# Kernel tuning notes

Measured on AMD Instinct MI355X. Metric: run time of the kernel, lower is better.

## Reference

```python
import jax, jax.numpy as jnp
import numpy as np
import math

# IPA hyperparameters (AlphaFold2 / ProtSeed defaults)
H, C, PQ, PV = 12, 16, 4, 8
CS, CZ = 384, 128
INF, EPS = 1e5, 1e-8
CAT = H * (CZ + C + 4 * PV)  # 2112


def setup_inputs() -> dict:
    key = jax.random.key(0)
    ks = jax.random.split(key, 20)
    B, N = 1, 512
    s = jax.random.normal(ks[0], (B, N, CS), jnp.float32)
    z = jax.random.normal(ks[1], (B, N, N, CZ), jnp.float32)
    # valid rotation matrices via QR of random gaussians
    rot = jnp.linalg.qr(jax.random.normal(ks[2], (B, N, 3, 3), jnp.float32))[0]
    trans = jax.random.normal(ks[3], (B, N, 3), jnp.float32)
    mask = jnp.ones((B, N), jnp.float32)
    sc = 0.02
    params = {
        'w_q': jax.random.normal(ks[4], (CS, H * C), jnp.float32) * sc,
        'b_q': jnp.zeros((H * C,), jnp.float32),
        'w_kv': jax.random.normal(ks[5], (CS, 2 * H * C), jnp.float32) * sc,
        'b_kv': jnp.zeros((2 * H * C,), jnp.float32),
        'w_qp': jax.random.normal(ks[6], (CS, H * PQ * 3), jnp.float32) * sc,
        'b_qp': jnp.zeros((H * PQ * 3,), jnp.float32),
        'w_kvp': jax.random.normal(ks[7], (CS, H * (PQ + PV) * 3), jnp.float32) * sc,
        'b_kvp': jnp.zeros((H * (PQ + PV) * 3,), jnp.float32),
        'w_b': jax.random.normal(ks[8], (CZ, H), jnp.float32) * sc,
        'b_b': jnp.zeros((H,), jnp.float32),
        'head_weights': jnp.full((H,), 0.5414, jnp.float32),  # softplus^-1(1)
        'w_out': jax.random.normal(ks[9], (CAT, CS), jnp.float32) * sc,
        'b_out': jnp.zeros((CS,), jnp.float32),
    }
    return {'s': s, 'z': z, 'rot': rot, 'trans': trans, 'mask': mask, **params}


def reference(s, z, rot, trans, mask, w_q, b_q, w_kv, b_kv, w_qp, b_qp,
              w_kvp, b_kvp, w_b, b_b, head_weights, w_out, b_out):
    B, N, _ = s.shape
    w_c = math.sqrt(1.0 / (3 * C))
    w_l = math.sqrt(1.0 / 3)
    w_p = math.sqrt(1.0 / (3 * (PQ * 9.0 / 2)))

    # scalar q/k/v: [B,N,H,C]
    q = (s @ w_q + b_q).reshape(B, N, H, C)
    kv = (s @ w_kv + b_kv).reshape(B, N, H, 2 * C)
    k, v = kv[..., :C], kv[..., C:]

    # point q/k/v in global frame. torch splits the projection into 3 chunks
    # (x,y,z) along the channel dim then stacks -> [B,N,H*P,3]
    def to_pts(w, b, p):
        pts = jnp.stack(jnp.split(s @ w + b, 3, axis=-1), axis=-1)  # [B,N,H*p,3]
        pts = jnp.einsum('bnij,bnpj->bnpi', rot, pts) + trans[:, :, None, :]
        return pts.reshape(B, N, H, p, 3)

    q_pts = to_pts(w_qp, b_qp, PQ)
    kv_pts = to_pts(w_kvp, b_kvp, PQ + PV)
    k_pts, v_pts = kv_pts[..., :PQ, :], kv_pts[..., PQ:, :]

    # pair bias [B,N,N,H]
    bias = z @ w_b + b_b

    # scalar attention logits [B,H,i,j]
    a = jnp.einsum('bihc,bjhc->bhij', q, k) * w_c
    a = a + w_l * jnp.transpose(bias, (0, 3, 1, 2))

    # point-distance term: [B,i,j,H,PQ]
    d2 = jnp.sum((q_pts[:, :, None] - k_pts[:, None]) ** 2, axis=-1)
    hw = jax.nn.softplus(head_weights) * w_p
    pt_att = -0.5 * jnp.sum(d2 * hw[None, None, None, :, None], axis=-1)  # [B,i,j,H]
    a = a + jnp.transpose(pt_att, (0, 3, 1, 2))

    sq_mask = INF * (mask[:, :, None] * mask[:, None, :] - 1.0)  # [B,i,j]
    a = jax.nn.softmax(a + sq_mask[:, None], axis=-1)  # [B,H,i,j]

    # scalar output [B,N,H*C]
    o = jnp.einsum('bhij,bjhc->bihc', a, v).reshape(B, N, H * C)

    # point output, mapped back to local frames: [B,i,H,PV,3]
    o_pt = jnp.einsum('bhij,bjhpx->bihpx', a, v_pts)
    o_pt = jnp.einsum('bnji,bnhpj->bnhpi', rot, o_pt - trans[:, :, None, None, :])
    o_pt_norm = jnp.sqrt(jnp.sum(o_pt ** 2, axis=-1) + EPS).reshape(B, N, H * PV)
    o_pt = o_pt.reshape(B, N, H * PV, 3)

    # pair output [B,N,H*CZ]
    o_pair = jnp.einsum('bhij,bijc->bihc', a, z).reshape(B, N, H * CZ)

    cat = jnp.concatenate(
        [o, o_pt[..., 0], o_pt[..., 1], o_pt[..., 2], o_pt_norm, o_pair], axis=-1)
    return cat @ w_out + b_out  # [B,N,C_s]
```

## Files before the change

### kernel.cpp

```cpp
#include <hip/hip_runtime.h>
#include <math.h>

#define NN 512
#define CSd 384
#define Hh 12
#define CATd 2112
#define KF_CHUNK 264
#define KF_SPLIT 8

__global__ void k_projgemm(const float* __restrict__ s,
                           const float* __restrict__ w_q, const float* __restrict__ b_q,
                           const float* __restrict__ w_kv, const float* __restrict__ b_kv,
                           const float* __restrict__ w_qp, const float* __restrict__ b_qp,
                           const float* __restrict__ w_kvp, const float* __restrict__ b_kvp,
                           float* __restrict__ proj)
{
  __shared__ float sT[384 * 40];
  const int t  = threadIdx.x;
  const int i0 = blockIdx.x * 32;
  const int c0 = blockIdx.y * 64;

  for (int u = t; u < 32 * 384; u += 256) {
    int row = u / 384, col = u % 384;
    sT[col * 40 + row] = s[(i0 + row) * CSd + col];
  }
  __syncthreads();

  const int c    = t & 63;
  const int rgrp = t >> 6;
  const int gc   = c0 + c;

  const float* wp;
  int stride;
  float bias;
  if (gc < 192)      { wp = w_q   + gc;         stride = 192; bias = b_q[gc]; }
  else if (gc < 576) { wp = w_kv  + (gc - 192); stride = 384; bias = b_kv[gc - 192]; }
  else if (gc < 720) { wp = w_qp  + (gc - 576); stride = 144; bias = b_qp[gc - 576]; }
  else               { wp = w_kvp + (gc - 720); stride = 432; bias = b_kvp[gc - 720]; }

  float acc[8];
#pragma unroll
  for (int j = 0; j < 8; j++) acc[j] = bias;

  const int r0 = rgrp * 8;
#pragma unroll 4
  for (int kk = 0; kk < 384; kk++) {
    float wv = *wp; wp += stride;
    const float4 a0 = *reinterpret_cast<const float4*>(&sT[kk * 40 + r0]);
    const float4 a1 = *reinterpret_cast<const float4*>(&sT[kk * 40 + r0 + 4]);
    acc[0] += a0.x * wv; acc[1] += a0.y * wv; acc[2] += a0.z * wv; acc[3] += a0.w * wv;
    acc[4] += a1.x * wv; acc[5] += a1.y * wv; acc[6] += a1.z * wv; acc[7] += a1.w * wv;
  }
#pragma unroll
  for (int j = 0; j < 8; j++)
    proj[(size_t)(i0 + r0 + j) * 1152 + gc] = acc[j];
}

__global__ void k_rot(const float* __restrict__ proj,
                      const float* __restrict__ rot, const float* __restrict__ trans,
                      float* __restrict__ q, float* __restrict__ kT, float* __restrict__ v,
                      float* __restrict__ qp, float* __restrict__ kpT, float* __restrict__ vp)
{
  __shared__ float ptsL[576];
  const int i = blockIdx.x, t = threadIdx.x;
  const float* pr = proj + (size_t)i * 1152;

  for (int u = t; u < 576; u += 256) ptsL[u] = pr[576 + u];

  for (int cI = t; cI < 576; cI += 256) {
    float pv = pr[cI];
    if (cI < 192) q[i * 192 + cI] = pv;
    else {
      int local = cI - 192, h = local >> 5, cc = local & 31;
      if (cc < 16) kT[(size_t)(h * 16 + cc) * NN + i] = pv;
      else         v[i * 192 + h * 16 + cc - 16] = pv;
    }
  }
  __syncthreads();

  for (int p = t; p < 192; p += 256) {
    float x, y, zz;
    if (p < 48) { x = ptsL[p]; y = ptsL[48 + p]; zz = ptsL[96 + p]; }
    else { int idx = p - 48; x = ptsL[144 + idx]; y = ptsL[288 + idx]; zz = ptsL[432 + idx]; }
    const float* Rm = rot + i * 9;
    const float* tr = trans + i * 3;
    float rx = Rm[0] * x + Rm[1] * y + Rm[2] * zz + tr[0];
    float ry = Rm[3] * x + Rm[4] * y + Rm[5] * zz + tr[1];
    float rz = Rm[6] * x + Rm[7] * y + Rm[8] * zz + tr[2];
    if (p < 48) {
      float* d = qp + ((size_t)i * 48 + p) * 3;
      d[0] = rx; d[1] = ry; d[2] = rz;
    } else {
      int idx = p - 48, h = idx / 12, pp = idx % 12;
      if (pp < 4) {
        size_t rbase = (size_t)((h * 4 + pp) * 3) * NN + i;
        kpT[rbase] = rx; kpT[rbase + NN] = ry; kpT[rbase + 2 * NN] = rz;
      } else {
        float* d = vp + ((size_t)i * 96 + h * 8 + pp - 4) * 3;
        d[0] = rx; d[1] = ry; d[2] = rz;
      }
    }
  }
}

__global__ void k_bias(const float* __restrict__ z, const float* __restrict__ w_b,
                       const float* __restrict__ b_b, const float* __restrict__ mask,
                       float* __restrict__ a)
{
  __shared__ float zL[64][129];
  __shared__ float wbL[128 * 12];
  const int t = threadIdx.x;
  const int row0 = blockIdx.x * 64;
  const int i = row0 >> 9;
  const int j0 = row0 & 511;

  for (int u = t; u < 1536; u += 256) wbL[u] = w_b[u];
  for (int u = t; u < 64 * 128; u += 256) zL[u >> 7][u & 127] = z[(size_t)row0 * 128 + u];
  __syncthreads();

  const int r = t & 63, hb = t >> 6;
  const float mi = mask[i], mj = mask[j0 + r];
  const float mterm = 100000.0f * (mi * mj - 1.0f);
  const float W_L = 0.57735026919f;
  const float* zr = zL[r];
  for (int hh = hb; hh < 12; hh += 4) {
    float acc = b_b[hh];
    for (int c = 0; c < 128; c++) acc += zr[c] * wbL[c * 12 + hh];
    a[((size_t)hh * NN + i) * NN + j0 + r] = W_L * acc + mterm;
  }
}

__global__ void k_attn(const float* __restrict__ q, const float* __restrict__ kT,
                       const float* __restrict__ qp, const float* __restrict__ kpT,
                       const float* __restrict__ hws, float* __restrict__ a)
{
  const int i = blockIdx.x, h = blockIdx.y, t = threadIdx.x;
  __shared__ float qL[16], qpL[12];
  __shared__ float red[2][4];
  if (t < 16) qL[t] = q[i * 192 + h * 16 + t];
  else if (t >= 32 && t < 44) qpL[t - 32] = qp[(size_t)i * 144 + h * 12 + (t - 32)];
  __syncthreads();

  const float hwv = 0.13608276348f * log1pf(expf(hws[h]));
  const float W_C = 0.14433756730f;
  const size_t base = ((size_t)h * NN + i) * NN;
  const int j = t * 2;

  float2 lg = *reinterpret_cast<const float2*>(&a[base + j]);

  float dx = 0.f, dy = 0.f;
#pragma unroll
  for (int c = 0; c < 16; c++) {
    float2 kv = *reinterpret_cast<const float2*>(&kT[(size_t)((h << 4) + c) * NN + j]);
    dx += qL[c] * kv.x; dy += qL[c] * kv.y;
  }
  float s2x = 0.f, s2y = 0.f;
#pragma unroll
  for (int pc = 0; pc < 12; pc++) {
    float2 kv = *reinterpret_cast<const float2*>(&kpT[(size_t)(h * 12 + pc) * NN + j]);
    float qv = qpL[pc];
    float ddx = qv - kv.x, ddy = qv - kv.y;
    s2x += ddx * ddx; s2y += ddy * ddy;
  }
  lg.x += W_C * dx - 0.5f * hwv * s2x;
  lg.y += W_C * dy - 0.5f * hwv * s2y;

  float m = fmaxf(lg.x, lg.y);
  for (int o = 1; o < 64; o <<= 1) m = fmaxf(m, __shfl_xor(m, o));
  if ((t & 63) == 0) red[0][t >> 6] = m;
  __syncthreads();
  m = fmaxf(fmaxf(red[0][0], red[0][1]), fmaxf(red[0][2], red[0][3]));
  float e0 = expf(lg.x - m), e1 = expf(lg.y - m);
  float sm = e0 + e1;
  for (int o = 1; o < 64; o <<= 1) sm += __shfl_xor(sm, o);
  if ((t & 63) == 0) red[1][t >> 6] = sm;
  __syncthreads();
  float inv = 1.0f / (red[1][0] + red[1][1] + red[1][2] + red[1][3]);
  float2 res = make_float2(e0 * inv, e1 * inv);
  *reinterpret_cast<float2*>(&a[base + j]) = res;
}

__global__ void k_out(const float* __restrict__ a, const float* __restrict__ v,
                      const float* __restrict__ vp, const float* __restrict__ z,
                      const float* __restrict__ rot, const float* __restrict__ trans,
                      float* __restrict__ cat)
{
  __shared__ float aL[12][513];
  __shared__ float optL[12][8][3];
  const int i = blockIdx.x, t = threadIdx.x;
  for (int u = t; u < 12 * 512; u += 512)
    aL[u >> 9][u & 511] = a[((size_t)(u >> 9) * NN + i) * NN + (u & 511)];
  __syncthreads();

  if (t < 192) {
    float acc = 0.f;
    const int h = t >> 4;
    for (int j = 0; j < 512; j++) acc += aL[h][j] * v[(size_t)j * 192 + t];
    cat[(size_t)i * CATd + t] = acc;
  } else if (t < 480) {
    int u = t - 192, h = u / 24;
    float acc = 0.f;
    for (int j = 0; j < 512; j++) acc += aL[h][j] * vp[(size_t)j * 288 + u];
    int pc = u % 24;
    optL[h][pc / 3][pc % 3] = acc;
  }
  __syncthreads();

  if (t < 96) {
    int h = t >> 3, p = t & 7;
    const float* Rm = rot + i * 9;
    const float* tr = trans + i * 3;
    float ox = optL[h][p][0] - tr[0];
    float oy = optL[h][p][1] - tr[1];
    float oz = optL[h][p][2] - tr[2];
    float rx = Rm[0] * ox + Rm[3] * oy + Rm[6] * oz;
    float ry = Rm[1] * ox + Rm[4] * oy + Rm[7] * oz;
    float rz = Rm[2] * ox + Rm[5] * oy + Rm[8] * oz;
    float nrm = sqrtf(rx * rx + ry * ry + rz * rz + 1e-8f);
    size_t b = (size_t)i * CATd;
    cat[b + 192 + t] = rx; cat[b + 288 + t] = ry;
    cat[b + 384 + t] = rz; cat[b + 480 + t] = nrm;
  }

  const int c = t & 127, hb = t >> 7;
  float a0 = 0.f, a1 = 0.f, a2 = 0.f;
  const float* zr = z + (size_t)i * 512 * 128 + c;
  for (int j = 0; j < 512; j++) {
    float zv = zr[(size_t)j * 128];
    a0 += aL[hb][j] * zv; a1 += aL[hb + 4][j] * zv; a2 += aL[hb + 8][j] * zv;
  }
  size_t b = (size_t)i * CATd + 576;
  cat[b + hb * 128 + c] = a0;
  cat[b + (hb + 4) * 128 + c] = a1;
  cat[b + (hb + 8) * 128 + c] = a2;
}

__global__ void k_final(const float* __restrict__ cat, const float* __restrict__ w_out,
                        float* __restrict__ part)
{
  __shared__ float sT[KF_CHUNK * 36];
  const int t  = threadIdx.x;
  const int i0 = blockIdx.x * 32;
  const int c0 = blockIdx.y * 64;
  const int k0 = blockIdx.z * KF_CHUNK;

  for (int u = t; u < 32 * KF_CHUNK; u += 256) {
    int row = u / KF_CHUNK, kk = u % KF_CHUNK;
    sT[kk * 36 + row] = cat[(size_t)(i0 + row) * CATd + k0 + kk];
  }
  __syncthreads();

  const int c    = t & 63;
  const int rgrp = t >> 6;
  const int r0   = rgrp * 8;
  const int gc   = c0 + c;

  float acc[8];
#pragma unroll
  for (int j = 0; j < 8; j++) acc[j] = 0.f;

  const float* wp = w_out + (size_t)k0 * 384 + gc;
#pragma unroll 4
  for (int kk = 0; kk < KF_CHUNK; kk++) {
    float wv = wp[(size_t)kk * 384];
    const float4 a0 = *reinterpret_cast<const float4*>(&sT[kk * 36 + r0]);
    const float4 a1 = *reinterpret_cast<const float4*>(&sT[kk * 36 + r0 + 4]);
    acc[0] += a0.x * wv; acc[1] += a0.y * wv; acc[2] += a0.z * wv; acc[3] += a0.w * wv;
    acc[4] += a1.x * wv; acc[5] += a1.y * wv; acc[6] += a1.z * wv; acc[7] += a1.w * wv;
  }

  float* pb = part + (size_t)blockIdx.z * NN * 384;
#pragma unroll
  for (int j = 0; j < 8; j++)
    pb[(size_t)(i0 + r0 + j) * 384 + gc] = acc[j];
}

__global__ void k_reduce(const float* __restrict__ part, const float* __restrict__ b_out,
                         float* __restrict__ out)
{
  const int idx = blockIdx.x * 256 + threadIdx.x;
  const int c = idx % 384;
  float acc = b_out[c];
#pragma unroll
  for (int ks = 0; ks < KF_SPLIT; ks++)
    acc += part[(size_t)ks * NN * 384 + idx];
  out[idx] = acc;
}

extern "C" void kernel_launch(void* const* d_in, const int* in_sizes, int n_in,
                              void* d_out, int out_size, void* d_ws, size_t ws_size,
                              hipStream_t stream) {
  const float* s      = (const float*)d_in[0];
  const float* z      = (const float*)d_in[1];
  const float* rot    = (const float*)d_in[2];
  const float* trans  = (const float*)d_in[3];
  const float* mask   = (const float*)d_in[4];
  const float* w_q    = (const float*)d_in[5];
  const float* b_q    = (const float*)d_in[6];
  const float* w_kv   = (const float*)d_in[7];
  const float* b_kv   = (const float*)d_in[8];
  const float* w_qp   = (const float*)d_in[9];
  const float* b_qp   = (const float*)d_in[10];
  const float* w_kvp  = (const float*)d_in[11];
  const float* b_kvp  = (const float*)d_in[12];
  const float* w_b    = (const float*)d_in[13];
  const float* b_b    = (const float*)d_in[14];
  const float* hws    = (const float*)d_in[15];
  const float* w_out  = (const float*)d_in[16];
  const float* b_out  = (const float*)d_in[17];
  float* out = (float*)d_out;

  float* ws  = (float*)d_ws;
  float* q   = ws;
  float* kT  = q  + 98304;
  float* v   = kT + 98304;
  float* qp  = v  + 98304;
  float* kpT = qp + 73728;
  float* vp  = kpT + 73728;
  float* a   = vp + 147456;
  float* cat = a  + 3145728;
  float* proj = a;
  float* part = a;

  k_projgemm<<<dim3(16, 18), 256, 0, stream>>>(s, w_q, b_q, w_kv, b_kv,
                                               w_qp, b_qp, w_kvp, b_kvp, proj);
  k_rot<<<512, 256, 0, stream>>>(proj, rot, trans, q, kT, v, qp, kpT, vp);
  k_bias<<<4096, 256, 0, stream>>>(z, w_b, b_b, mask, a);
  k_attn<<<dim3(512, 12), 256, 0, stream>>>(q, kT, qp, kpT, hws, a);
  k_out<<<512, 512, 0, stream>>>(a, v, vp, z, rot, trans, cat);
  k_final<<<dim3(16, 6, KF_SPLIT), 256, 0, stream>>>(cat, w_out, part);
  k_reduce<<<768, 256, 0, stream>>>(part, b_out, out);
}
```

Measured before the change: 209.4 us.

## Split channel and j reductions across threads in bias and pair-output kernels

k_bias now loads z with float4 into padded shared memory and transposes w_b. Each thread reduces a 32-channel slice for all 12 heads, and the four slices are summed through shared memory, so z is read from LDS once rather than once per head group. In k_out, each z element is loaded from global memory once and used for all 12 heads: the four thread groups each take a quarter of the j range and their partials are combined through a new shared buffer. This cuts the repeated z traffic but adds about 25KB of shared memory and an extra sync, which may lower occupancy.

```diff
diff --git a/kernel.cpp b/kernel.cpp
--- a/kernel.cpp
+++ b/kernel.cpp
@@ -107,26 +107,54 @@
                        const float* __restrict__ b_b, const float* __restrict__ mask,
                        float* __restrict__ a)
 {
-  __shared__ float zL[64][129];
-  __shared__ float wbL[128 * 12];
+  __shared__ float zL[64 * 132];
+  __shared__ float wT[12 * 128];
+  __shared__ float red[4][64][13];
   const int t = threadIdx.x;
   const int row0 = blockIdx.x * 64;
   const int i = row0 >> 9;
   const int j0 = row0 & 511;
 
-  for (int u = t; u < 1536; u += 256) wbL[u] = w_b[u];
-  for (int u = t; u < 64 * 128; u += 256) zL[u >> 7][u & 127] = z[(size_t)row0 * 128 + u];
-  __syncthreads();
-
-  const int r = t & 63, hb = t >> 6;
-  const float mi = mask[i], mj = mask[j0 + r];
+  for (int u = t; u < 1536; u += 256) {
+    int h = u >> 7, c = u & 127;
+    wT[u] = w_b[c * 12 + h];
+  }
+  const float4* z4 = reinterpret_cast<const float4*>(z + (size_t)row0 * 128);
+  for (int u = t; u < 64 * 32; u += 256) {
+    int r = u >> 5, c4 = u & 31;
+    *reinterpret_cast<float4*>(&zL[r * 132 + c4 * 4]) = z4[u];
+  }
+  __syncthreads();
+
+  const int r = t & 63, cq = t >> 6;
+  float4 zr[8];
+#pragma unroll
+  for (int i4 = 0; i4 < 8; i4++)
+    zr[i4] = *reinterpret_cast<const float4*>(&zL[r * 132 + cq * 32 + i4 * 4]);
+
+  float acc[12];
+#pragma unroll
+  for (int h = 0; h < 12; h++) {
+    float sv = 0.f;
+#pragma unroll
+    for (int i4 = 0; i4 < 8; i4++) {
+      const float4 w = *reinterpret_cast<const float4*>(&wT[h * 128 + cq * 32 + i4 * 4]);
+      sv += zr[i4].x * w.x + zr[i4].y * w.y + zr[i4].z * w.z + zr[i4].w * w.w;
+    }
+    acc[h] = sv;
+  }
+#pragma unroll
+  for (int h = 0; h < 12; h++) red[cq][r][h] = acc[h];
+  __syncthreads();
+
+  const int rr = t & 63, hg = t >> 6;
+  const float mi = mask[i], mj = mask[j0 + rr];
   const float mterm = 100000.0f * (mi * mj - 1.0f);
   const float W_L = 0.57735026919f;
-  const float* zr = zL[r];
-  for (int hh = hb; hh < 12; hh += 4) {
-    float acc = b_b[hh];
-    for (int c = 0; c < 128; c++) acc += zr[c] * wbL[c * 12 + hh];
-    a[((size_t)hh * NN + i) * NN + j0 + r] = W_L * acc + mterm;
+#pragma unroll
+  for (int h = hg * 3; h < hg * 3 + 3; h++) {
+    float sv = b_b[h] + red[0][rr][h] + red[1][rr][h] + red[2][rr][h] + red[3][rr][h];
+    a[((size_t)h * NN + i) * NN + j0 + rr] = W_L * sv + mterm;
   }
 }
 
@@ -187,9 +215,27 @@
 {
   __shared__ float aL[12][513];
   __shared__ float optL[12][8][3];
+  __shared__ float redp[4][12][129];
   const int i = blockIdx.x, t = threadIdx.x;
   for (int u = t; u < 12 * 512; u += 512)
     aL[u >> 9][u & 511] = a[((size_t)(u >> 9) * NN + i) * NN + (u & 511)];
+  __syncthreads();
+
+  {
+    const int c = t & 127, jq = t >> 7;
+    float pa[12];
+#pragma unroll
+    for (int h = 0; h < 12; h++) pa[h] = 0.f;
+    const float* zr = z + (size_t)i * 65536 + c;
+    const int jend = jq * 128 + 128;
+    for (int j = jq * 128; j < jend; j++) {
+      float zv = zr[(size_t)j * 128];
+#pragma unroll
+      for (int h = 0; h < 12; h++) pa[h] += aL[h][j] * zv;
+    }
+#pragma unroll
+    for (int h = 0; h < 12; h++) redp[jq][h][c] = pa[h];
+  }
   __syncthreads();
 
   if (t < 192) {
@@ -222,17 +268,13 @@
     cat[b + 384 + t] = rz; cat[b + 480 + t] = nrm;
   }
 
-  const int c = t & 127, hb = t >> 7;
-  float a0 = 0.f, a1 = 0.f, a2 = 0.f;
-  const float* zr = z + (size_t)i * 512 * 128 + c;
-  for (int j = 0; j < 512; j++) {
-    float zv = zr[(size_t)j * 128];
-    a0 += aL[hb][j] * zv; a1 += aL[hb + 4][j] * zv; a2 += aL[hb + 8][j] * zv;
-  }
-  size_t b = (size_t)i * CATd + 576;
-  cat[b + hb * 128 + c] = a0;
-  cat[b + (hb + 4) * 128 + c] = a1;
-  cat[b + (hb + 8) * 128 + c] = a2;
+#pragma unroll
+  for (int kph = 0; kph < 3; kph++) {
+    int e = t + kph * 512;
+    int h = e >> 7, c = e & 127;
+    float sv = redp[0][h][c] + redp[1][h][c] + redp[2][h][c] + redp[3][h][c];
+    cat[(size_t)i * CATd + 576 + e] = sv;
+  }
 }
 
 __global__ void k_final(const float* __restrict__ cat, const float* __restrict__ w_out,
```

New measurement: 199.8 us. 4.6% less time.
